# Kernel optimization log

Measured on AMD Instinct MI355X. Metric: run time of the kernel, lower is better.

## Reference

```python
import jax, jax.numpy as jnp
import numpy as np

NUM_CLASSES = 81
N_ROIS = 100000
N_GT = 512
ROIS_PER_IMAGE = 256
FG_ROIS_PER_IMAGE = 128  # fg_fraction * rois_per_image
FG_THRESH = 0.5
BG_HI = 0.5
BG_LO = 0.1


def _make_boxes(key, n, img=1024.0):
    k1, k2, k3, k4 = jax.random.split(key, 4)
    x1 = jax.random.uniform(k1, (n,)) * (img - 160.0)
    y1 = jax.random.uniform(k2, (n,)) * (img - 160.0)
    w = 16.0 + jax.random.uniform(k3, (n,)) * 112.0
    h = 16.0 + jax.random.uniform(k4, (n,)) * 112.0
    return jnp.stack([x1, y1, x1 + w, y1 + h], axis=1)


def setup_inputs() -> dict:
    key = jax.random.key(0)
    kg, kc, kn, kr, ks = jax.random.split(key, 5)
    gt_xyxy = _make_boxes(kg, N_GT)
    gt_cls = jax.random.randint(kc, (N_GT, 1), 1, NUM_CLASSES).astype(jnp.float32)
    gt_boxes = jnp.concatenate([gt_xyxy, gt_cls], axis=1)
    # first block of proposals = jittered gt boxes so fg samples exist
    n_jit = 4096
    reps = int(np.ceil(n_jit / N_GT))
    jit_base = jnp.tile(gt_xyxy, (reps, 1))[:n_jit]
    noise = (jax.random.uniform(kn, (n_jit, 4)) - 0.5) * 12.0
    jit_boxes = jit_base + noise
    rand_boxes = _make_boxes(kr, N_ROIS - n_jit)
    boxes = jnp.concatenate([jit_boxes, rand_boxes], axis=0)
    rpn_rois = jnp.concatenate([jnp.zeros((N_ROIS, 1), jnp.float32), boxes], axis=1)
    rpn_scores = jax.random.uniform(ks, (N_ROIS, 1), dtype=jnp.float32)
    return {"rpn_rois": rpn_rois, "rpn_scores": rpn_scores, "gt_boxes": gt_boxes}


def _bbox_overlaps(b1, b2):
    # b1 [N,4], b2 [G,4] -> IoU [N,G] with +1 pixel convention
    x1a, y1a, x2a, y2a = b1[:, 0], b1[:, 1], b1[:, 2], b1[:, 3]
    x1b, y1b, x2b, y2b = b2[:, 0], b2[:, 1], b2[:, 2], b2[:, 3]
    iw = jnp.maximum(0.0, jnp.minimum(x2a[:, None], x2b[None, :]) - jnp.maximum(x1a[:, None], x1b[None, :]) + 1.0)
    ih = jnp.maximum(0.0, jnp.minimum(y2a[:, None], y2b[None, :]) - jnp.maximum(y1a[:, None], y1b[None, :]) + 1.0)
    inter = iw * ih
    a1 = (x2a - x1a + 1.0) * (y2a - y1a + 1.0)
    a2 = (x2b - x1b + 1.0) * (y2b - y1b + 1.0)
    union = a1[:, None] + a2[None, :] - inter
    return jnp.where(inter == 0.0, 0.0, inter / union)


def _bbox_transform(ex, gt):
    ew = ex[:, 2] - ex[:, 0] + 1.0
    eh = ex[:, 3] - ex[:, 1] + 1.0
    ecx = ex[:, 0] + 0.5 * ew
    ecy = ex[:, 1] + 0.5 * eh
    gw = gt[:, 2] - gt[:, 0] + 1.0
    gh = gt[:, 3] - gt[:, 1] + 1.0
    gcx = gt[:, 0] + 0.5 * gw
    gcy = gt[:, 1] + 0.5 * gh
    return jnp.stack([(gcx - ecx) / ew, (gcy - ecy) / eh, jnp.log(gw / ew), jnp.log(gh / eh)], axis=1)


def _forward(rpn_rois, rpn_scores, gt_boxes):
    means = jnp.array([0.0, 0.0, 0.0, 0.0], jnp.float32)
    stds = jnp.array([0.1, 0.1, 0.2, 0.2], jnp.float32)
    k1, k2, k3 = jax.random.split(jax.random.key(42), 3)
    n = rpn_rois.shape[0]
    overlaps = _bbox_overlaps(rpn_rois[:, 1:5], gt_boxes[:, :4])  # [N,G]
    gt_assignment = jnp.argmax(overlaps, axis=1)  # [N]
    max_overlaps = jnp.max(overlaps, axis=1)      # [N]
    fg_mask = max_overlaps >= FG_THRESH
    bg_mask = (max_overlaps < BG_HI) & (max_overlaps >= BG_LO)
    # shuffled candidate orderings: random key for candidates, +2 sentinel pushes rest to the back
    fg_order = jnp.argsort(jnp.where(fg_mask, jax.random.uniform(k1, (n,)), 2.0))
    bg_order = jnp.argsort(jnp.where(bg_mask, jax.random.uniform(k2, (n,)), 2.0))
    fg_count = jnp.minimum(FG_ROIS_PER_IMAGE, jnp.sum(fg_mask))
    bg_count = jnp.minimum(ROIS_PER_IMAGE - fg_count, jnp.sum(bg_mask))
    pos = jnp.arange(ROIS_PER_IMAGE)
    sel = jnp.where(pos < fg_count, fg_order[pos], bg_order[jnp.maximum(pos - fg_count, 0)])
    # fill any shortfall by re-sampling uniformly from the fg+bg picks
    n_samp = fg_count + bg_count
    n_safe = jnp.maximum(n_samp, 1)
    dup = (jax.random.uniform(k3, (ROIS_PER_IMAGE,)) * n_safe).astype(jnp.int32)
    sel = jnp.where(pos < n_samp, sel, sel[dup])
    gt_ids = gt_assignment[sel]
    labels = gt_boxes[gt_ids, 4]
    fmax = max_overlaps[sel]
    labels = jnp.where((fmax < BG_HI) & (fmax >= BG_LO), 0.0, labels)
    rois = rpn_rois[sel]                 # [256,5]
    roi_scores = rpn_scores[sel].reshape(-1)
    targets = _bbox_transform(rois[:, 1:5], gt_boxes[gt_ids, :4])
    targets = (targets - means) / stds
    # expand compact (cls,tx,ty,tw,th) into N x 4K, nonzero only at own-class slot
    cls = labels.astype(jnp.int32)
    valid = (labels > 0).astype(jnp.float32)[:, None]
    rows = pos[:, None]
    cols = cls[:, None] * 4 + jnp.arange(4)[None, :]
    zeros4k = jnp.zeros((ROIS_PER_IMAGE, 4 * NUM_CLASSES), jnp.float32)
    bbox_targets = zeros4k.at[rows, cols].set(targets * valid)
    bbox_inside = zeros4k.at[rows, cols].set(jnp.ones((1, 4), jnp.float32) * valid)
    bbox_outside = (bbox_inside > 0).astype(jnp.float32)
    return rois, roi_scores, labels, bbox_targets, bbox_inside, bbox_outside


def reference(rpn_rois, rpn_scores, gt_boxes):
    return _forward(rpn_rois, rpn_scores, gt_boxes)
```

## Files before the change

kernel.cpp:

```cpp
#include <hip/hip_runtime.h>
#include <stdint.h>

__host__ __device__ inline void tf2x32(uint32_t ks0, uint32_t ks1, uint32_t x0, uint32_t x1,
                                       uint32_t& o0, uint32_t& o1) {
  uint32_t ks2 = ks0 ^ ks1 ^ 0x1BD11BDAu;
#define TFR(r) { x0 += x1; x1 = (x1 << (r)) | (x1 >> (32 - (r))); x1 ^= x0; }
  x0 += ks0; x1 += ks1;
  TFR(13) TFR(15) TFR(26) TFR(6)
  x0 += ks1; x1 += ks2 + 1u;
  TFR(17) TFR(29) TFR(16) TFR(24)
  x0 += ks2; x1 += ks0 + 2u;
  TFR(13) TFR(15) TFR(26) TFR(6)
  x0 += ks0; x1 += ks1 + 3u;
  TFR(17) TFR(29) TFR(16) TFR(24)
  x0 += ks1; x1 += ks2 + 4u;
  TFR(13) TFR(15) TFR(26) TFR(6)
  x0 += ks2; x1 += ks0 + 5u;
#undef TFR
  o0 = x0; o1 = x1;
}

__device__ inline float bits_to_unif(uint32_t b) {
  return __uint_as_float((b >> 9) | 0x3F800000u) - 1.0f;
}

__device__ inline uint32_t jbits(int v, uint32_t ka, uint32_t kb, uint32_t i, uint32_t n) {
  uint32_t o0, o1;
  if (v == 2) {
    uint32_t h = (n + 1) >> 1;
    if (i < h) {
      uint32_t xh = (i + h < n) ? (i + h) : 0u;
      tf2x32(ka, kb, i, xh, o0, o1);
      return o0;
    }
    tf2x32(ka, kb, i - h, i, o0, o1);
    return o1;
  }
  tf2x32(ka, kb, 0u, i, o0, o1);
  return (v == 0) ? o0 : (o0 ^ o1);
}

#define NGT_MAX      512
#define ROIS_PER_IMG 256
#define FG_PER_IMG   128
#define NCOLS        324
#define NB           1024
#define CAND_CAP     2048
#define GT_SPLIT     4

#define OFF_SCORES 1280
#define OFF_LABELS 1536
#define OFF_BIG    1792
#define BIGN       (ROIS_PER_IMG * NCOLS)

#define WS_MAXOV   0
#define WS_GTASGN  400000
#define WS_HIST    800000
#define WS_CANDF   808192
#define WS_CANDB   824576
#define WS_META    840960
#define WS_CLS     841024
#define WS_T       842048

__global__ void __launch_bounds__(1024) k_detect(const float* __restrict__ scores,
                                                 int n, int* __restrict__ meta,
                                                 int* __restrict__ hist) {
  int tid = threadIdx.x;
  hist[tid] = 0;
  hist[NB + tid] = 0;
  if (tid == 11 || tid == 12) meta[tid] = 0;

  if (tid < 64) {
    uint32_t pa, pb; tf2x32(0u, 0u, 0u, 4u, pa, pb);
    uint32_t t0, t1, q0, q1;
    tf2x32(0u, 0u, 3u, 8u, t0, t1);
    tf2x32(0u, 0u, 4u, 9u, q0, q1);
    uint32_t la = t1, lb = q1;

    bool m0 = false, m1 = false, m2 = false;
    if (tid < 16) {
      uint32_t sref = __float_as_uint(scores[tid]);
      uint32_t o0, o1; tf2x32(pa, pb, 0u, (uint32_t)tid, o0, o1);
      m0 = (__float_as_uint(bits_to_unif(o0)) == sref);
      m1 = (__float_as_uint(bits_to_unif(o0 ^ o1)) == sref);
      uint32_t h = (uint32_t)(n >> 1);
      uint32_t c0, c1; tf2x32(la, lb, (uint32_t)tid, (uint32_t)tid + h, c0, c1);
      m2 = (__float_as_uint(bits_to_unif(c0)) == sref);
    }
    int n0 = __popcll(__ballot(m0));
    int n1 = __popcll(__ballot(m1));
    int n2 = __popcll(__ballot(m2));
    if (tid == 0) {
      int v = (n1 >= n0 && n1 >= n2) ? 1 : ((n0 >= n2) ? 0 : 2);
      meta[0] = v;
      uint32_t K[6];
      if (v == 2) {
        uint32_t a0, a1, b0, b1, c0, c1;
        tf2x32(0u, 42u, 0u, 3u, a0, a1);
        tf2x32(0u, 42u, 1u, 4u, b0, b1);
        tf2x32(0u, 42u, 2u, 5u, c0, c1);
        K[0] = a0; K[1] = b0; K[2] = c0; K[3] = a1; K[4] = b1; K[5] = c1;
      } else {
        tf2x32(0u, 42u, 0u, 0u, K[0], K[1]);
        tf2x32(0u, 42u, 0u, 1u, K[2], K[3]);
        tf2x32(0u, 42u, 0u, 2u, K[4], K[5]);
      }
      for (int j = 0; j < 6; ++j) meta[1 + j] = (int)K[j];
    }
  }
}

__global__ void __launch_bounds__(256) k_iou(const float* __restrict__ rois,
                                             const float* __restrict__ gt,
                                             int n, int ngt,
                                             float* __restrict__ maxov,
                                             int* __restrict__ gtasgn,
                                             int* __restrict__ hist,
                                             const int* __restrict__ meta) {
#pragma clang fp contract(off)
  __shared__ float4 sgt4[NGT_MAX];
  __shared__ float sarea[NGT_MAX];
  __shared__ float sbest[GT_SPLIT][64];
  __shared__ int   sbi[GT_SPLIT][64];
  __shared__ int smeta[8];
  const int tid = threadIdx.x;
  if (tid < 8) smeta[tid] = meta[tid];
  for (int g = tid; g < ngt; g += blockDim.x) {
    float x1 = gt[g * 5 + 0], y1 = gt[g * 5 + 1];
    float x2 = gt[g * 5 + 2], y2 = gt[g * 5 + 3];
    sgt4[g] = make_float4(x1, y1, x2, y2);
    sarea[g] = (x2 - x1 + 1.0f) * (y2 - y1 + 1.0f);
  }
  __syncthreads();

  const int wave = tid >> 6;
  const int lane = tid & 63;
  const int i = blockIdx.x * 64 + lane;
  const bool valid = (i < n);

  float ax1 = 0, ay1 = 0, ax2 = 0, ay2 = 0, a1 = 1;
  if (valid) {
    ax1 = rois[i * 5 + 1]; ay1 = rois[i * 5 + 2];
    ax2 = rois[i * 5 + 3]; ay2 = rois[i * 5 + 4];
    a1 = (ax2 - ax1 + 1.0f) * (ay2 - ay1 + 1.0f);
  }

  const int csz = (ngt + GT_SPLIT - 1) / GT_SPLIT;
  const int g0 = wave * csz;
  const int g1 = min(ngt, g0 + csz);

  float best = -1.0f; int bi = 0;
  for (int j = g0; j < g1; ++j) {
    float4 g4 = sgt4[j];
    float a2 = sarea[j];
    float iw = fmaxf(0.0f, fminf(ax2, g4.z) - fmaxf(ax1, g4.x) + 1.0f);
    float ih = fmaxf(0.0f, fminf(ay2, g4.w) - fmaxf(ay1, g4.y) + 1.0f);
    float inter = iw * ih;
    float uni = a1 + a2 - inter;
    float iou = (inter == 0.0f) ? 0.0f : (inter / uni);
    if (iou > best) { best = iou; bi = j; }
  }
  sbest[wave][lane] = best;
  sbi[wave][lane] = bi;
  __syncthreads();

  if (wave == 0) {
    for (int w = 1; w < GT_SPLIT; ++w) {
      float ob = sbest[w][lane];
      int oi = sbi[w][lane];
      if (ob > best || (ob == best && oi < bi)) { best = ob; bi = oi; }
    }
    if (valid) {
      maxov[i] = best;
      gtasgn[i] = bi;
      if (best >= 0.1f) {
        const int v = smeta[0];
        const bool fg = (best >= 0.5f);
        uint32_t ka = (uint32_t)(fg ? smeta[1] : smeta[3]);
        uint32_t kb = (uint32_t)(fg ? smeta[2] : smeta[4]);
        uint32_t b = jbits(v, ka, kb, (uint32_t)i, (uint32_t)n);
        int bk = min(NB - 1, (int)(bits_to_unif(b) * (float)NB));
        atomicAdd(&hist[(fg ? 0 : NB) + bk], 1);
      }
    }
  }
}

__global__ void __launch_bounds__(1024) k_scan(const int* __restrict__ hist,
                                               int* __restrict__ meta) {
  __shared__ int hf[NB], hb[NB];
  const int tid = threadIdx.x;
  hf[tid] = hist[tid];
  hb[tid] = hist[NB + tid];
  __syncthreads();
  for (int s = 1; s < NB; s <<= 1) {
    int tf_ = hf[tid] + ((tid >= s) ? hf[tid - s] : 0);
    int tb_ = hb[tid] + ((tid >= s) ? hb[tid - s] : 0);
    __syncthreads();
    hf[tid] = tf_; hb[tid] = tb_;
    __syncthreads();
  }
  const int fg_count = min(FG_PER_IMG, hf[NB - 1]);
  const int bg_count = min(ROIS_PER_IMG - fg_count, hb[NB - 1]);
  if (tid == 0) {
    meta[9] = fg_count;
    meta[10] = bg_count;
    if (fg_count == 0) meta[7] = -1;
    if (bg_count == 0) meta[8] = -1;
  }
  if (fg_count > 0 && hf[tid] >= fg_count && (tid == 0 || hf[tid - 1] < fg_count)) meta[7] = tid;
  if (bg_count > 0 && hb[tid] >= bg_count && (tid == 0 || hb[tid - 1] < bg_count)) meta[8] = tid;
}

__global__ void k_collect(const float* __restrict__ maxov, int n,
                          int* __restrict__ meta,
                          unsigned long long* __restrict__ candf,
                          unsigned long long* __restrict__ candb) {
  __shared__ int smeta[9];
  if (threadIdx.x < 9) smeta[threadIdx.x] = meta[threadIdx.x];
  __syncthreads();
  const int i = blockIdx.x * blockDim.x + threadIdx.x;
  if (i >= n) return;
  const int v = smeta[0];
  const int Bf = smeta[7], Bb = smeta[8];
  float m = maxov[i];
  if (m >= 0.5f) {
    if (Bf >= 0) {
      uint32_t b = jbits(v, (uint32_t)smeta[1], (uint32_t)smeta[2], (uint32_t)i, (uint32_t)n);
      if (min(NB - 1, (int)(bits_to_unif(b) * (float)NB)) <= Bf) {
        int p = atomicAdd(&meta[11], 1);
        if (p < CAND_CAP) candf[p] = ((unsigned long long)(b >> 9) << 32) | (unsigned)i;
      }
    }
  } else if (m >= 0.1f) {
    if (Bb >= 0) {
      uint32_t b = jbits(v, (uint32_t)smeta[3], (uint32_t)smeta[4], (uint32_t)i, (uint32_t)n);
      if (min(NB - 1, (int)(bits_to_unif(b) * (float)NB)) <= Bb) {
        int p = atomicAdd(&meta[12], 1);
        if (p < CAND_CAP) candb[p] = ((unsigned long long)(b >> 9) << 32) | (unsigned)i;
      }
    }
  }
}

__device__ inline void bitonic(unsigned long long* buf, int nelem, int tid, int nthr) {
  for (int k = 2; k <= nelem; k <<= 1)
    for (int j = k >> 1; j > 0; j >>= 1) {
      for (int i = tid; i < nelem; i += nthr) {
        int l = i ^ j;
        if (l > i) {
          unsigned long long a = buf[i], b = buf[l];
          bool swap_ = ((i & k) == 0) ? (a > b) : (a < b);
          if (swap_) { buf[i] = b; buf[l] = a; }
        }
      }
      __syncthreads();
    }
}

__global__ void __launch_bounds__(1024) k_pick(
    const float* __restrict__ rois, const float* __restrict__ scores,
    const float* __restrict__ gt,
    const float* __restrict__ maxov, const int* __restrict__ gtasgn,
    const int* __restrict__ meta,
    const unsigned long long* __restrict__ gcandf,
    const unsigned long long* __restrict__ gcandb,
    float* __restrict__ out, int* __restrict__ ws_cls, float* __restrict__ ws_t) {
#pragma clang fp contract(off)
  __shared__ unsigned long long candf[CAND_CAP], candb[CAND_CAP];
  __shared__ int sel[ROIS_PER_IMG];
  __shared__ int smeta[13];
  const int tid = threadIdx.x;
  const int nthr = 1024;
  if (tid < 13) smeta[tid] = meta[tid];
  __syncthreads();
  const int v = smeta[0];
  const uint32_t k3a = (uint32_t)smeta[5], k3b = (uint32_t)smeta[6];
  const int fg_count = smeta[9], bg_count = smeta[10];
  const int Mf = min(smeta[11], CAND_CAP);
  const int Mb = min(smeta[12], CAND_CAP);

  int nf = 1; while (nf < Mf) nf <<= 1;
  int nb = 1; while (nb < Mb) nb <<= 1;
  for (int i = tid; i < nf; i += nthr) candf[i] = (i < Mf) ? gcandf[i] : ~0ull;
  for (int i = tid; i < nb; i += nthr) candb[i] = (i < Mb) ? gcandb[i] : ~0ull;
  __syncthreads();

  bitonic(candf, nf, tid, nthr);
  bitonic(candb, nb, tid, nthr);
  __syncthreads();

  if (tid < fg_count) sel[tid] = (int)(candf[tid] & 0xFFFFFFFFull);
  if (tid < bg_count) sel[fg_count + tid] = (int)(candb[tid] & 0xFFFFFFFFull);
  __syncthreads();

  const int n_samp = fg_count + bg_count;
  if (tid < ROIS_PER_IMG && tid >= n_samp) {
    if (n_samp > 0) {
      uint32_t b3 = jbits(v, k3a, k3b, (uint32_t)tid, (uint32_t)ROIS_PER_IMG);
      int d = (int)(bits_to_unif(b3) * (float)n_samp);
      d = min(d, n_samp - 1);
      sel[tid] = sel[d];
    } else {
      sel[tid] = 0;
    }
  }
  __syncthreads();

  if (tid < ROIS_PER_IMG) {
    int i = sel[tid];
    int g = gtasgn[i];
    float fmax = maxov[i];
    float label = gt[g * 5 + 4];
    if (fmax < 0.5f && fmax >= 0.1f) label = 0.0f;

    for (int c = 0; c < 5; ++c) out[tid * 5 + c] = rois[i * 5 + c];
    out[OFF_SCORES + tid] = scores[i];
    out[OFF_LABELS + tid] = label;

    float ex0 = rois[i * 5 + 1], ey0 = rois[i * 5 + 2];
    float ex1 = rois[i * 5 + 3], ey1 = rois[i * 5 + 4];
    float gx0 = gt[g * 5 + 0], gy0 = gt[g * 5 + 1];
    float gx1 = gt[g * 5 + 2], gy1 = gt[g * 5 + 3];
    float ew = ex1 - ex0 + 1.0f, eh = ey1 - ey0 + 1.0f;
    float ecx = ex0 + 0.5f * ew, ecy = ey0 + 0.5f * eh;
    float gw = gx1 - gx0 + 1.0f, gh = gy1 - gy0 + 1.0f;
    float gcx = gx0 + 0.5f * gw, gcy = gy0 + 0.5f * gh;
    float t0 = ((gcx - ecx) / ew) / 0.1f;
    float t1 = ((gcy - ecy) / eh) / 0.1f;
    float t2 = logf(gw / ew) / 0.2f;
    float t3 = logf(gh / eh) / 0.2f;

    float valid = (label > 0.0f) ? 1.0f : 0.0f;
    int cls = (int)label;
    ws_cls[tid] = (valid > 0.0f) ? cls : -1;
    ws_t[tid * 4 + 0] = t0 * valid;
    ws_t[tid * 4 + 1] = t1 * valid;
    ws_t[tid * 4 + 2] = t2 * valid;
    ws_t[tid * 4 + 3] = t3 * valid;
  }
}

__global__ void k_out(const int* __restrict__ ws_cls, const float* __restrict__ ws_t,
                      float* __restrict__ out) {
  int e = blockIdx.x * blockDim.x + threadIdx.x;
  if (e >= BIGN) return;
  int r = e / NCOLS, c = e % NCOLS;
  int cls = ws_cls[r];
  float tv = 0.0f, iv = 0.0f;
  if (cls >= 0) {
    int c0 = cls * 4;
    if (c >= c0 && c < c0 + 4) { tv = ws_t[r * 4 + (c - c0)]; iv = 1.0f; }
  }
  out[OFF_BIG + e] = tv;
  out[OFF_BIG + BIGN + e] = iv;
  out[OFF_BIG + 2 * BIGN + e] = iv;
}

extern "C" void kernel_launch(void* const* d_in, const int* in_sizes, int n_in,
                              void* d_out, int out_size, void* d_ws, size_t ws_size,
                              hipStream_t stream) {
  const float* rois   = (const float*)d_in[0];
  const float* scores = (const float*)d_in[1];
  const float* gt     = (const float*)d_in[2];
  float* out = (float*)d_out;

  const int n   = in_sizes[0] / 5;
  const int ngt = in_sizes[2] / 5;

  char* ws = (char*)d_ws;
  float* maxov  = (float*)(ws + WS_MAXOV);
  int*   gtasgn = (int*)(ws + WS_GTASGN);
  int*   hist   = (int*)(ws + WS_HIST);
  unsigned long long* candf = (unsigned long long*)(ws + WS_CANDF);
  unsigned long long* candb = (unsigned long long*)(ws + WS_CANDB);
  int*   meta   = (int*)(ws + WS_META);
  int*   wcls   = (int*)(ws + WS_CLS);
  float* wt     = (float*)(ws + WS_T);

  k_detect<<<1, 1024, 0, stream>>>(scores, n, meta, hist);
  k_iou<<<(n + 63) / 64, 256, 0, stream>>>(rois, gt, n, ngt, maxov, gtasgn, hist, meta);
  k_scan<<<1, 1024, 0, stream>>>(hist, meta);
  k_collect<<<(n + 255) / 256, 256, 0, stream>>>(maxov, n, meta, candf, candb);
  k_pick<<<1, 1024, 0, stream>>>(rois, scores, gt, maxov, gtasgn, meta,
                                 candf, candb, out, wcls, wt);
  k_out<<<(BIGN + 255) / 256, 256, 0, stream>>>(wcls, wt, out);
}
```

Baseline: 88.04 us.

## Split IoU into overlap-mask pass and sparse divide pass over overlapping GTs

The IoU kernel first builds 64-bit masks of which GT boxes overlap each ROI using only min/max tests, then runs the area/divide work only for the set bits. This avoids a division and select for every ROI-GT pair, since most pairs do not overlap. The histogram bucket is now taken from the top 10 random bits with a shift instead of a float conversion and multiply. The change also clears more meta slots in the detect kernel. The cost is a second, divergent loop over set bits and a fixed fast path that assumes 128 GTs per wave.

```diff
diff --git a/kernel.cpp b/kernel.cpp
--- a/kernel.cpp
+++ b/kernel.cpp
@@ -40,13 +40,15 @@
   return (v == 0) ? o0 : (o0 ^ o1);
 }
 
+__device__ inline int jbucket(uint32_t b) { return (int)(b >> 22); }
+
 #define NGT_MAX      512
 #define ROIS_PER_IMG 256
 #define FG_PER_IMG   128
 #define NCOLS        324
 #define NB           1024
 #define CAND_CAP     2048
-#define GT_SPLIT     4
+#define WAVES        4
 
 #define OFF_SCORES 1280
 #define OFF_LABELS 1536
@@ -63,12 +65,13 @@
 #define WS_T       842048
 
 __global__ void __launch_bounds__(1024) k_detect(const float* __restrict__ scores,
-                                                 int n, int* __restrict__ meta,
+                                                 int n,
+                                                 int* __restrict__ meta,
                                                  int* __restrict__ hist) {
   int tid = threadIdx.x;
   hist[tid] = 0;
   hist[NB + tid] = 0;
-  if (tid == 11 || tid == 12) meta[tid] = 0;
+  if (tid >= 7 && tid <= 13) meta[tid] = 0;
 
   if (tid < 64) {
     uint32_t pa, pb; tf2x32(0u, 0u, 0u, 4u, pa, pb);
@@ -120,11 +123,13 @@
 #pragma clang fp contract(off)
   __shared__ float4 sgt4[NGT_MAX];
   __shared__ float sarea[NGT_MAX];
-  __shared__ float sbest[GT_SPLIT][64];
-  __shared__ int   sbi[GT_SPLIT][64];
-  __shared__ int smeta[8];
+  __shared__ float sbest[WAVES][64];
+  __shared__ int   sbi[WAVES][64];
+  __shared__ int   smeta[7];
   const int tid = threadIdx.x;
-  if (tid < 8) smeta[tid] = meta[tid];
+  const int wave = tid >> 6;
+  const int lane = tid & 63;
+  if (tid < 7) smeta[tid] = meta[tid];
   for (int g = tid; g < ngt; g += blockDim.x) {
     float x1 = gt[g * 5 + 0], y1 = gt[g * 5 + 1];
     float x2 = gt[g * 5 + 2], y2 = gt[g * 5 + 3];
@@ -133,55 +138,96 @@
   }
   __syncthreads();
 
-  const int wave = tid >> 6;
-  const int lane = tid & 63;
   const int i = blockIdx.x * 64 + lane;
   const bool valid = (i < n);
 
-  float ax1 = 0, ay1 = 0, ax2 = 0, ay2 = 0, a1 = 1;
+  float ax1 = 1e30f, ay1 = 1e30f, ax2 = -1e30f, ay2 = -1e30f, a1 = 1.0f;
   if (valid) {
     ax1 = rois[i * 5 + 1]; ay1 = rois[i * 5 + 2];
     ax2 = rois[i * 5 + 3]; ay2 = rois[i * 5 + 4];
     a1 = (ax2 - ax1 + 1.0f) * (ay2 - ay1 + 1.0f);
   }
 
-  const int csz = (ngt + GT_SPLIT - 1) / GT_SPLIT;
+  const int csz = (ngt + WAVES - 1) / WAVES;
   const int g0 = wave * csz;
-  const int g1 = min(ngt, g0 + csz);
-
-  float best = -1.0f; int bi = 0;
-  for (int j = g0; j < g1; ++j) {
-    float4 g4 = sgt4[j];
-    float a2 = sarea[j];
-    float iw = fmaxf(0.0f, fminf(ax2, g4.z) - fmaxf(ax1, g4.x) + 1.0f);
-    float ih = fmaxf(0.0f, fminf(ay2, g4.w) - fmaxf(ay1, g4.y) + 1.0f);
+  const int cnt = max(0, min(ngt, g0 + csz) - g0);
+
+  unsigned long long m0 = 0ull, m1 = 0ull;
+  if (cnt == 128) {
+#pragma unroll 8
+    for (int jj = 0; jj < 64; ++jj) {
+      float4 G = sgt4[g0 + jj];
+      float iw = fminf(ax2, G.z) - fmaxf(ax1, G.x) + 1.0f;
+      float ih = fminf(ay2, G.w) - fmaxf(ay1, G.y) + 1.0f;
+      if (iw > 0.0f && ih > 0.0f) m0 |= (1ull << jj);
+    }
+#pragma unroll 8
+    for (int jj = 0; jj < 64; ++jj) {
+      float4 G = sgt4[g0 + 64 + jj];
+      float iw = fminf(ax2, G.z) - fmaxf(ax1, G.x) + 1.0f;
+      float ih = fminf(ay2, G.w) - fmaxf(ay1, G.y) + 1.0f;
+      if (iw > 0.0f && ih > 0.0f) m1 |= (1ull << jj);
+    }
+  } else {
+    const int c0 = min(cnt, 64);
+    for (int jj = 0; jj < c0; ++jj) {
+      float4 G = sgt4[g0 + jj];
+      float iw = fminf(ax2, G.z) - fmaxf(ax1, G.x) + 1.0f;
+      float ih = fminf(ay2, G.w) - fmaxf(ay1, G.y) + 1.0f;
+      if (iw > 0.0f && ih > 0.0f) m0 |= (1ull << jj);
+    }
+    for (int jj = 64; jj < cnt; ++jj) {
+      float4 G = sgt4[g0 + jj];
+      float iw = fminf(ax2, G.z) - fmaxf(ax1, G.x) + 1.0f;
+      float ih = fminf(ay2, G.w) - fmaxf(ay1, G.y) + 1.0f;
+      if (iw > 0.0f && ih > 0.0f) m1 |= (1ull << (jj - 64));
+    }
+  }
+
+  float best = 0.0f; int bi = 0;
+  while (m0) {
+    int jj = __builtin_ctzll(m0);
+    m0 &= m0 - 1ull;
+    int j = g0 + jj;
+    float4 G = sgt4[j];
+    float iw = fminf(ax2, G.z) - fmaxf(ax1, G.x) + 1.0f;
+    float ih = fminf(ay2, G.w) - fmaxf(ay1, G.y) + 1.0f;
     float inter = iw * ih;
-    float uni = a1 + a2 - inter;
-    float iou = (inter == 0.0f) ? 0.0f : (inter / uni);
+    float uni = a1 + sarea[j] - inter;
+    float iou = inter / uni;
+    if (iou > best) { best = iou; bi = j; }
+  }
+  while (m1) {
+    int jj = __builtin_ctzll(m1);
+    m1 &= m1 - 1ull;
+    int j = g0 + 64 + jj;
+    float4 G = sgt4[j];
+    float iw = fminf(ax2, G.z) - fmaxf(ax1, G.x) + 1.0f;
+    float ih = fminf(ay2, G.w) - fmaxf(ay1, G.y) + 1.0f;
+    float inter = iw * ih;
+    float uni = a1 + sarea[j] - inter;
+    float iou = inter / uni;
     if (iou > best) { best = iou; bi = j; }
   }
   sbest[wave][lane] = best;
   sbi[wave][lane] = bi;
   __syncthreads();
 
-  if (wave == 0) {
-    for (int w = 1; w < GT_SPLIT; ++w) {
+  if (wave == 0 && valid) {
+    for (int w = 1; w < WAVES; ++w) {
       float ob = sbest[w][lane];
       int oi = sbi[w][lane];
       if (ob > best || (ob == best && oi < bi)) { best = ob; bi = oi; }
     }
-    if (valid) {
-      maxov[i] = best;
-      gtasgn[i] = bi;
-      if (best >= 0.1f) {
-        const int v = smeta[0];
-        const bool fg = (best >= 0.5f);
-        uint32_t ka = (uint32_t)(fg ? smeta[1] : smeta[3]);
-        uint32_t kb = (uint32_t)(fg ? smeta[2] : smeta[4]);
-        uint32_t b = jbits(v, ka, kb, (uint32_t)i, (uint32_t)n);
-        int bk = min(NB - 1, (int)(bits_to_unif(b) * (float)NB));
-        atomicAdd(&hist[(fg ? 0 : NB) + bk], 1);
-      }
+    maxov[i] = best;
+    gtasgn[i] = bi;
+    if (best >= 0.1f) {
+      const int v = smeta[0];
+      const bool fg = (best >= 0.5f);
+      uint32_t ka = (uint32_t)(fg ? smeta[1] : smeta[3]);
+      uint32_t kb = (uint32_t)(fg ? smeta[2] : smeta[4]);
+      uint32_t b = jbits(v, ka, kb, (uint32_t)i, (uint32_t)n);
+      atomicAdd(&hist[(fg ? 0 : NB) + jbucket(b)], 1);
     }
   }
 }
@@ -227,7 +273,7 @@
   if (m >= 0.5f) {
     if (Bf >= 0) {
       uint32_t b = jbits(v, (uint32_t)smeta[1], (uint32_t)smeta[2], (uint32_t)i, (uint32_t)n);
-      if (min(NB - 1, (int)(bits_to_unif(b) * (float)NB)) <= Bf) {
+      if (jbucket(b) <= Bf) {
         int p = atomicAdd(&meta[11], 1);
         if (p < CAND_CAP) candf[p] = ((unsigned long long)(b >> 9) << 32) | (unsigned)i;
       }
@@ -235,7 +281,7 @@
   } else if (m >= 0.1f) {
     if (Bb >= 0) {
       uint32_t b = jbits(v, (uint32_t)smeta[3], (uint32_t)smeta[4], (uint32_t)i, (uint32_t)n);
-      if (min(NB - 1, (int)(bits_to_unif(b) * (float)NB)) <= Bb) {
+      if (jbucket(b) <= Bb) {
         int p = atomicAdd(&meta[12], 1);
         if (p < CAND_CAP) candb[p] = ((unsigned long long)(b >> 9) << 32) | (unsigned)i;
       }
```

Result: faster. 71.04 us (-19.3%).

## Prune IoU search with a uniform spatial grid over ground-truth boxes

Applied to the files above, without the earlier changes.

Bins the ground-truth boxes into a 16x16 grid in the detect kernel, sorted by cell with prefix-sum offsets and the maximum gt width and height. The IoU kernel then tests each ROI only against gt boxes in cells that can overlap it, instead of all 512. Each thread now handles one ROI, so the cross-wave reduction is gone. The output-expansion kernel is vectorised to float4 stores and the histogram bucket is computed directly from the random bits. The risks are load imbalance from uneven cell occupancy and exact tie-breaking and IoU parity with the brute-force scan.

```diff
diff --git a/kernel.cpp b/kernel.cpp
--- a/kernel.cpp
+++ b/kernel.cpp
@@ -40,13 +40,16 @@
   return (v == 0) ? o0 : (o0 ^ o1);
 }
 
+__device__ inline int jbucket(uint32_t b) { return (int)(b >> 22); }
+
 #define NGT_MAX      512
 #define ROIS_PER_IMG 256
 #define FG_PER_IMG   128
 #define NCOLS        324
 #define NB           1024
 #define CAND_CAP     2048
-#define GT_SPLIT     4
+#define NCELL        16
+#define CELL_INV     0.015625f
 
 #define OFF_SCORES 1280
 #define OFF_LABELS 1536
@@ -61,14 +64,75 @@
 #define WS_META    840960
 #define WS_CLS     841024
 #define WS_T       842048
+#define WS_GT8     846144
+#define WS_CSTART  862528
+#define WS_CLIST   863568
 
 __global__ void __launch_bounds__(1024) k_detect(const float* __restrict__ scores,
-                                                 int n, int* __restrict__ meta,
-                                                 int* __restrict__ hist) {
-  int tid = threadIdx.x;
+                                                 const float* __restrict__ gt,
+                                                 int n, int ngt,
+                                                 int* __restrict__ meta,
+                                                 int* __restrict__ hist,
+                                                 float* __restrict__ gt8,
+                                                 int* __restrict__ cellStart,
+                                                 int* __restrict__ cellList) {
+#pragma clang fp contract(off)
+  __shared__ int ccnt[NCELL * NCELL];
+  __shared__ int cs[NCELL * NCELL];
+  __shared__ int crun[NCELL * NCELL];
+  __shared__ int scell[NGT_MAX];
+  __shared__ int cmax[2];
+  const int tid = threadIdx.x;
   hist[tid] = 0;
   hist[NB + tid] = 0;
-  if (tid == 11 || tid == 12) meta[tid] = 0;
+  if (tid >= 7 && tid <= 13) meta[tid] = 0;
+  if (tid < NCELL * NCELL) ccnt[tid] = 0;
+  if (tid < 2) cmax[tid] = 0;
+  __syncthreads();
+
+  const int ng = min(ngt, NGT_MAX);
+  if (tid < ng) {
+    float x1 = gt[tid * 5 + 0], y1 = gt[tid * 5 + 1];
+    float x2 = gt[tid * 5 + 2], y2 = gt[tid * 5 + 3];
+    gt8[tid * 8 + 0] = x1; gt8[tid * 8 + 1] = y1;
+    gt8[tid * 8 + 2] = x2; gt8[tid * 8 + 3] = y2;
+    gt8[tid * 8 + 4] = (x2 - x1 + 1.0f) * (y2 - y1 + 1.0f);
+    gt8[tid * 8 + 5] = gt[tid * 5 + 4];
+    gt8[tid * 8 + 6] = 0.0f; gt8[tid * 8 + 7] = 0.0f;
+    int cx = min(NCELL - 1, max(0, (int)floorf(x1 * CELL_INV)));
+    int cy = min(NCELL - 1, max(0, (int)floorf(y1 * CELL_INV)));
+    int cell = cy * NCELL + cx;
+    scell[tid] = cell;
+    atomicAdd(&ccnt[cell], 1);
+    atomicMax(&cmax[0], __float_as_int(x2 - x1));
+    atomicMax(&cmax[1], __float_as_int(y2 - y1));
+  }
+  __syncthreads();
+
+  if (tid < NCELL * NCELL) cs[tid] = ccnt[tid];
+  __syncthreads();
+  for (int s = 1; s < NCELL * NCELL; s <<= 1) {
+    int v = 0;
+    if (tid < NCELL * NCELL) v = cs[tid] + ((tid >= s) ? cs[tid - s] : 0);
+    __syncthreads();
+    if (tid < NCELL * NCELL) cs[tid] = v;
+    __syncthreads();
+  }
+  if (tid < NCELL * NCELL) {
+    int off = cs[tid] - ccnt[tid];
+    crun[tid] = off;
+    cellStart[tid] = off;
+  }
+  if (tid == 0) {
+    cellStart[NCELL * NCELL] = ng;
+    meta[14] = cmax[0];
+    meta[15] = cmax[1];
+  }
+  __syncthreads();
+  if (tid < ng) {
+    int pos = atomicAdd(&crun[scell[tid]], 1);
+    cellList[pos] = tid;
+  }
 
   if (tid < 64) {
     uint32_t pa, pb; tf2x32(0u, 0u, 0u, 4u, pa, pb);
@@ -111,7 +175,9 @@
 }
 
 __global__ void __launch_bounds__(256) k_iou(const float* __restrict__ rois,
-                                             const float* __restrict__ gt,
+                                             const float* __restrict__ gt8,
+                                             const int* __restrict__ gcellStart,
+                                             const int* __restrict__ gcellList,
                                              int n, int ngt,
                                              float* __restrict__ maxov,
                                              int* __restrict__ gtasgn,
@@ -120,69 +186,68 @@
 #pragma clang fp contract(off)
   __shared__ float4 sgt4[NGT_MAX];
   __shared__ float sarea[NGT_MAX];
-  __shared__ float sbest[GT_SPLIT][64];
-  __shared__ int   sbi[GT_SPLIT][64];
-  __shared__ int smeta[8];
+  __shared__ int scs[NCELL * NCELL + 1];
+  __shared__ int scl[NGT_MAX];
+  __shared__ int smeta[16];
   const int tid = threadIdx.x;
-  if (tid < 8) smeta[tid] = meta[tid];
-  for (int g = tid; g < ngt; g += blockDim.x) {
-    float x1 = gt[g * 5 + 0], y1 = gt[g * 5 + 1];
-    float x2 = gt[g * 5 + 2], y2 = gt[g * 5 + 3];
-    sgt4[g] = make_float4(x1, y1, x2, y2);
-    sarea[g] = (x2 - x1 + 1.0f) * (y2 - y1 + 1.0f);
-  }
-  __syncthreads();
-
-  const int wave = tid >> 6;
-  const int lane = tid & 63;
-  const int i = blockIdx.x * 64 + lane;
-  const bool valid = (i < n);
-
-  float ax1 = 0, ay1 = 0, ax2 = 0, ay2 = 0, a1 = 1;
-  if (valid) {
-    ax1 = rois[i * 5 + 1]; ay1 = rois[i * 5 + 2];
-    ax2 = rois[i * 5 + 3]; ay2 = rois[i * 5 + 4];
-    a1 = (ax2 - ax1 + 1.0f) * (ay2 - ay1 + 1.0f);
-  }
-
-  const int csz = (ngt + GT_SPLIT - 1) / GT_SPLIT;
-  const int g0 = wave * csz;
-  const int g1 = min(ngt, g0 + csz);
-
-  float best = -1.0f; int bi = 0;
-  for (int j = g0; j < g1; ++j) {
-    float4 g4 = sgt4[j];
-    float a2 = sarea[j];
-    float iw = fmaxf(0.0f, fminf(ax2, g4.z) - fmaxf(ax1, g4.x) + 1.0f);
-    float ih = fmaxf(0.0f, fminf(ay2, g4.w) - fmaxf(ay1, g4.y) + 1.0f);
-    float inter = iw * ih;
-    float uni = a1 + a2 - inter;
-    float iou = (inter == 0.0f) ? 0.0f : (inter / uni);
-    if (iou > best) { best = iou; bi = j; }
-  }
-  sbest[wave][lane] = best;
-  sbi[wave][lane] = bi;
-  __syncthreads();
-
-  if (wave == 0) {
-    for (int w = 1; w < GT_SPLIT; ++w) {
-      float ob = sbest[w][lane];
-      int oi = sbi[w][lane];
-      if (ob > best || (ob == best && oi < bi)) { best = ob; bi = oi; }
-    }
-    if (valid) {
-      maxov[i] = best;
-      gtasgn[i] = bi;
-      if (best >= 0.1f) {
-        const int v = smeta[0];
-        const bool fg = (best >= 0.5f);
-        uint32_t ka = (uint32_t)(fg ? smeta[1] : smeta[3]);
-        uint32_t kb = (uint32_t)(fg ? smeta[2] : smeta[4]);
-        uint32_t b = jbits(v, ka, kb, (uint32_t)i, (uint32_t)n);
-        int bk = min(NB - 1, (int)(bits_to_unif(b) * (float)NB));
-        atomicAdd(&hist[(fg ? 0 : NB) + bk], 1);
+  if (tid < 16) smeta[tid] = meta[tid];
+  const int ng = min(ngt, NGT_MAX);
+  {
+    const float4* g4p = (const float4*)gt8;
+    for (int g = tid; g < ng; g += 256) {
+      float4 box = g4p[2 * g];
+      float4 ext = g4p[2 * g + 1];
+      sgt4[g] = box;
+      sarea[g] = ext.x;
+      scl[g] = gcellList[g];
+    }
+    for (int c = tid; c < NCELL * NCELL + 1; c += 256) scs[c] = gcellStart[c];
+  }
+  __syncthreads();
+
+  const int i = blockIdx.x * 256 + tid;
+  if (i >= n) return;
+
+  const float x1 = rois[i * 5 + 1], y1 = rois[i * 5 + 2];
+  const float x2 = rois[i * 5 + 3], y2 = rois[i * 5 + 4];
+  const float a1 = (x2 - x1 + 1.0f) * (y2 - y1 + 1.0f);
+  const float maxGWm1 = __int_as_float(smeta[14]);
+  const float maxGHm1 = __int_as_float(smeta[15]);
+
+  const int cx0 = max(0, (int)floorf((x1 - 1.5f - maxGWm1) * CELL_INV));
+  const int cx1 = min(NCELL - 1, (int)floorf((x2 + 1.5f) * CELL_INV));
+  const int cy0 = max(0, (int)floorf((y1 - 1.5f - maxGHm1) * CELL_INV));
+  const int cy1 = min(NCELL - 1, (int)floorf((y2 + 1.5f) * CELL_INV));
+
+  float best = 0.0f; int bi = 0;
+  for (int cy = cy0; cy <= cy1; ++cy) {
+    for (int cx = cx0; cx <= cx1; ++cx) {
+      const int cell = cy * NCELL + cx;
+      const int k0 = scs[cell], k1 = scs[cell + 1];
+      for (int k = k0; k < k1; ++k) {
+        const int j = scl[k];
+        const float4 G = sgt4[j];
+        float iw = fminf(x2, G.z) - fmaxf(x1, G.x) + 1.0f;
+        float ih = fminf(y2, G.w) - fmaxf(y1, G.y) + 1.0f;
+        if (iw > 0.0f && ih > 0.0f) {
+          float inter = iw * ih;
+          float uni = a1 + sarea[j] - inter;
+          float iou = inter / uni;
+          if (iou > best || (iou == best && j < bi)) { best = iou; bi = j; }
+        }
       }
     }
+  }
+
+  maxov[i] = best;
+  gtasgn[i] = bi;
+  if (best >= 0.1f) {
+    const int v = smeta[0];
+    const bool fg = (best >= 0.5f);
+    uint32_t ka = (uint32_t)(fg ? smeta[1] : smeta[3]);
+    uint32_t kb = (uint32_t)(fg ? smeta[2] : smeta[4]);
+    uint32_t b = jbits(v, ka, kb, (uint32_t)i, (uint32_t)n);
+    atomicAdd(&hist[(fg ? 0 : NB) + jbucket(b)], 1);
   }
 }
 
@@ -227,7 +292,7 @@
   if (m >= 0.5f) {
     if (Bf >= 0) {
       uint32_t b = jbits(v, (uint32_t)smeta[1], (uint32_t)smeta[2], (uint32_t)i, (uint32_t)n);
-      if (min(NB - 1, (int)(bits_to_unif(b) * (float)NB)) <= Bf) {
+      if (jbucket(b) <= Bf) {
         int p = atomicAdd(&meta[11], 1);
         if (p < CAND_CAP) candf[p] = ((unsigned long long)(b >> 9) << 32) | (unsigned)i;
       }
@@ -235,7 +300,7 @@
   } else if (m >= 0.1f) {
     if (Bb >= 0) {
       uint32_t b = jbits(v, (uint32_t)smeta[3], (uint32_t)smeta[4], (uint32_t)i, (uint32_t)n);
-      if (min(NB - 1, (int)(bits_to_unif(b) * (float)NB)) <= Bb) {
+      if (jbucket(b) <= Bb) {
         int p = atomicAdd(&meta[12], 1);
         if (p < CAND_CAP) candb[p] = ((unsigned long long)(b >> 9) << 32) | (unsigned)i;
       }
@@ -343,18 +408,24 @@
 
 __global__ void k_out(const int* __restrict__ ws_cls, const float* __restrict__ ws_t,
                       float* __restrict__ out) {
-  int e = blockIdx.x * blockDim.x + threadIdx.x;
-  if (e >= BIGN) return;
-  int r = e / NCOLS, c = e % NCOLS;
+  const int QROW = NCOLS / 4;
+  const int TOT4 = ROIS_PER_IMG * QROW;
+  int e4 = blockIdx.x * blockDim.x + threadIdx.x;
+  if (e4 >= TOT4) return;
+  int r = e4 / QROW, q = e4 - r * QROW;
   int cls = ws_cls[r];
-  float tv = 0.0f, iv = 0.0f;
-  if (cls >= 0) {
-    int c0 = cls * 4;
-    if (c >= c0 && c < c0 + 4) { tv = ws_t[r * 4 + (c - c0)]; iv = 1.0f; }
-  }
-  out[OFF_BIG + e] = tv;
-  out[OFF_BIG + BIGN + e] = iv;
-  out[OFF_BIG + 2 * BIGN + e] = iv;
+  float4 tv = make_float4(0.f, 0.f, 0.f, 0.f);
+  float4 iv = make_float4(0.f, 0.f, 0.f, 0.f);
+  if (cls >= 0 && q == cls) {
+    tv = *(const float4*)(ws_t + r * 4);
+    iv = make_float4(1.f, 1.f, 1.f, 1.f);
+  }
+  float4* o0 = (float4*)(out + OFF_BIG);
+  float4* o1 = (float4*)(out + OFF_BIG + BIGN);
+  float4* o2 = (float4*)(out + OFF_BIG + 2 * BIGN);
+  o0[e4] = tv;
+  o1[e4] = iv;
+  o2[e4] = iv;
 }
 
 extern "C" void kernel_launch(void* const* d_in, const int* in_sizes, int n_in,
@@ -377,12 +448,16 @@
   int*   meta   = (int*)(ws + WS_META);
   int*   wcls   = (int*)(ws + WS_CLS);
   float* wt     = (float*)(ws + WS_T);
-
-  k_detect<<<1, 1024, 0, stream>>>(scores, n, meta, hist);
-  k_iou<<<(n + 63) / 64, 256, 0, stream>>>(rois, gt, n, ngt, maxov, gtasgn, hist, meta);
+  float* gt8    = (float*)(ws + WS_GT8);
+  int*   cstart = (int*)(ws + WS_CSTART);
+  int*   clist  = (int*)(ws + WS_CLIST);
+
+  k_detect<<<1, 1024, 0, stream>>>(scores, gt, n, ngt, meta, hist, gt8, cstart, clist);
+  k_iou<<<(n + 255) / 256, 256, 0, stream>>>(rois, gt8, cstart, clist, n, ngt,
+                                             maxov, gtasgn, hist, meta);
   k_scan<<<1, 1024, 0, stream>>>(hist, meta);
   k_collect<<<(n + 255) / 256, 256, 0, stream>>>(maxov, n, meta, candf, candb);
   k_pick<<<1, 1024, 0, stream>>>(rois, scores, gt, maxov, gtasgn, meta,
                                  candf, candb, out, wcls, wt);
-  k_out<<<(BIGN + 255) / 256, 256, 0, stream>>>(wcls, wt, out);
-}
+  k_out<<<(ROIS_PER_IMG * (NCOLS / 4) + 255) / 256, 256, 0, stream>>>(wcls, wt, out);
+}
```

New measurement: 92.95 us. 1.06x slower.
